# Performance work log

Measured on AMD Instinct MI355X. Metric: run time of the kernel, lower is better.

## Reference

```python
import jax, jax.numpy as jnp
import numpy as np

B, L = 16, 1024
D_MODEL, D_STATE, N_LAYERS = 256, 16, 2
FRAME_DIM, N_FRAMES, N_ACT = 115, 4, 19
GNN_H, GNN_K, ACT_EMB, GRID, N_PLAYERS = 32, 6, 16, 5, 22


def _ln(x, g, b, eps=1e-5):
    m = x.mean(-1, keepdims=True)
    v = ((x - m) ** 2).mean(-1, keepdims=True)
    return (x - m) / jnp.sqrt(v + eps) * g + b


def _kan(x, g, b, Wsp, Wbase, bias, beta):
    # x: [N, FRAME_DIM]
    grid = jnp.linspace(-1.0, 1.0, GRID)
    x = _ln(x, g, b)
    bta = jnp.clip(beta, 0.5, 6.0)
    basis = jnp.exp(-((x[..., None] - grid) ** 2) * bta)  # [N, I, G]
    # original: einsum('bdig,oid->bod').sum(-1) with basis dim d==1 broadcast
    # == sum over i, g (basis) and d (spline grid axis)
    spline = jnp.einsum('big,oid->bo', basis, Wsp)
    base = x @ Wbase.T
    return base + spline + bias


def _graph(fc, fp):
    # fc, fp: [N, 115] current / previous frame
    Bn = fc.shape[0]
    ball = fc[:, :2]
    lp = fc[:, 3:25].reshape(Bn, 11, 2)
    rp = fc[:, 25:47].reshape(Bn, 11, 2)
    lpp = fp[:, 3:25].reshape(Bn, 11, 2)
    rpp = fp[:, 25:47].reshape(Bn, 11, 2)
    pos = jnp.concatenate([lp, rp], 1)           # [N, 22, 2]
    posp = jnp.concatenate([lpp, rpp], 1)
    vel = pos - posp
    team = jnp.concatenate([jnp.zeros((Bn, 11, 1)), jnp.ones((Bn, 11, 1))], 1)
    bd = jnp.sqrt(((pos - ball[:, None, :]) ** 2).sum(-1, keepdims=True))
    prox = jnp.exp(-bd * 2)
    lc = lp.mean(1, keepdims=True)
    rc = rp.mean(1, keepdims=True)
    tc = jnp.concatenate([jnp.broadcast_to(lc, (Bn, 11, 2)),
                          jnp.broadcast_to(rc, (Bn, 11, 2))], 1)
    nodes = jnp.concatenate([pos, vel, team, prox, pos - tc], -1)  # [N, 22, 8]
    eye = jnp.eye(N_PLAYERS)
    d = jnp.sqrt(((pos[:, :, None, :] - pos[:, None, :, :]) ** 2).sum(-1)) + eye * 1e6
    _, idx = jax.lax.top_k(-d, GNN_K)
    adj = jax.nn.one_hot(idx, N_PLAYERS).sum(-2)
    adj = jnp.minimum(adj + eye, 1.0)
    adj = adj / jnp.clip(adj.sum(-1, keepdims=True), 1.0, None)
    # the torch model computes the graph under no_grad
    return jax.lax.stop_gradient(nodes), jax.lax.stop_gradient(adj)


def _s6(x, h0, lng, lnb, Win, Wdt, bdt, Alog, WB, WC, Dp, Wout):
    Bn, Ln, Dm = x.shape
    h0 = h0.reshape(Bn, Dm, D_STATE)
    xn = _ln(x, lng, lnb)
    xz = xn @ Win.T
    x_in, z = jnp.split(xz, 2, axis=-1)
    dt = jax.nn.softplus(x_in @ Wdt.T + bdt)     # [B, L, D]
    A = -jnp.exp(Alog)                            # [D, N]
    Bt = x_in @ WB.T                              # [B, L, N]
    Ct = x_in @ WC.T

    def step(h, inp):
        dt_t, x_t, B_t, C_t = inp                 # [B,D],[B,D],[B,N],[B,N]
        dA = jnp.exp(dt_t[:, :, None] * A)        # [B, D, N]
        h = dA * h + (dt_t * x_t)[:, :, None] * B_t[:, None, :]
        y = (h * C_t[:, None, :]).sum(-1)         # [B, D]
        return h, y

    hL, ys = jax.lax.scan(step, h0, (dt.swapaxes(0, 1), x_in.swapaxes(0, 1),
                                     Bt.swapaxes(0, 1), Ct.swapaxes(0, 1)))
    y = ys.swapaxes(0, 1)
    ssm = y * jax.nn.silu(z) + x_in * Dp
    return x + ssm @ Wout.T, hL.reshape(Bn, -1)


def setup_inputs() -> dict:
    key = jax.random.key(0)
    ks = iter(jax.random.split(key, 80))

    def nrm(shape, s=0.05):
        return jax.random.normal(next(ks), shape, dtype=jnp.float32) * s

    inp = {}
    inp['obs'] = jax.random.normal(next(ks), (B, L, N_FRAMES, FRAME_DIM), dtype=jnp.float32)
    inp['prev_actions'] = jax.random.randint(next(ks), (B, L), 0, N_ACT)
    inp['h0_0'] = jnp.zeros((B, D_MODEL * D_STATE), jnp.float32)
    inp['h0_1'] = jnp.zeros((B, D_MODEL * D_STATE), jnp.float32)
    inp['kan_ln_g'] = jnp.ones((FRAME_DIM,), jnp.float32)
    inp['kan_ln_b'] = jnp.zeros((FRAME_DIM,), jnp.float32)
    inp['kan_spline'] = nrm((D_MODEL, FRAME_DIM, GRID), 0.1)
    inp['kan_scale'] = jnp.ones((D_MODEL, FRAME_DIM), jnp.float32)
    inp['kan_bias'] = jnp.zeros((D_MODEL,), jnp.float32)
    inp['kan_beta'] = jnp.full((1,), 2.0, jnp.float32)
    inp['fn_g'] = jnp.ones((D_MODEL,), jnp.float32)
    inp['fn_b'] = jnp.zeros((D_MODEL,), jnp.float32)
    inp['gnn_W'] = nrm((GNN_H, 8))
    inp['edge_w'] = jnp.full((1,), 0.5, jnp.float32)
    inp['act_emb'] = nrm((N_ACT, ACT_EMB), 1.0)
    inp['W_ip'] = nrm((D_MODEL, D_MODEL + GNN_H + ACT_EMB))
    inp['b_ip'] = jnp.zeros((D_MODEL,), jnp.float32)
    for i in range(N_LAYERS):
        p = 'm%d_' % i
        inp[p + 'lng'] = jnp.ones((D_MODEL,), jnp.float32)
        inp[p + 'lnb'] = jnp.zeros((D_MODEL,), jnp.float32)
        inp[p + 'Win'] = nrm((2 * D_MODEL, D_MODEL))
        inp[p + 'Wdt'] = nrm((D_MODEL, D_MODEL))
        inp[p + 'bdt'] = jnp.zeros((D_MODEL,), jnp.float32)
        inp[p + 'Alog'] = jax.random.uniform(next(ks), (D_MODEL, D_STATE),
                                             minval=-3.0, maxval=-1.0, dtype=jnp.float32)
        inp[p + 'WB'] = nrm((D_STATE, D_MODEL))
        inp[p + 'WC'] = nrm((D_STATE, D_MODEL))
        inp[p + 'D'] = jnp.ones((D_MODEL,), jnp.float32)
        inp[p + 'Wout'] = nrm((D_MODEL, D_MODEL))
    inp['fl_g'] = jnp.ones((D_MODEL,), jnp.float32)
    inp['fl_b'] = jnp.zeros((D_MODEL,), jnp.float32)
    inp['pW1'] = nrm((128, D_MODEL)); inp['pb1'] = jnp.zeros((128,), jnp.float32)
    inp['pW2'] = nrm((N_ACT, 128)); inp['pb2'] = jnp.zeros((N_ACT,), jnp.float32)
    inp['vW1'] = nrm((64, D_MODEL)); inp['vb1'] = jnp.zeros((64,), jnp.float32)
    inp['vW2'] = nrm((1, 64)); inp['vb2'] = jnp.zeros((1,), jnp.float32)
    return inp


def reference(obs, prev_actions, h0_0, h0_1,
              kan_ln_g, kan_ln_b, kan_spline, kan_scale, kan_bias, kan_beta,
              fn_g, fn_b, gnn_W, edge_w, act_emb, W_ip, b_ip,
              m0_lng, m0_lnb, m0_Win, m0_Wdt, m0_bdt, m0_Alog, m0_WB, m0_WC, m0_D, m0_Wout,
              m1_lng, m1_lnb, m1_Win, m1_Wdt, m1_bdt, m1_Alog, m1_WB, m1_WC, m1_D, m1_Wout,
              fl_g, fl_b, pW1, pb1, pW2, pb2, vW1, vb1, vW2, vb2):
    BL = B * L
    # frame encoder (KAN) over all frames of all timesteps
    flat = obs.reshape(BL * N_FRAMES, FRAME_DIM)
    fe = _kan(flat, kan_ln_g, kan_ln_b, kan_spline, kan_scale, kan_bias, kan_beta)
    fe = jax.nn.relu(_ln(fe.reshape(BL, N_FRAMES, D_MODEL), fn_g, fn_b))
    feat = fe.mean(1)                                   # [BL, D]
    # GNN on last two frames
    fc = obs[:, :, -1, :].reshape(BL, FRAME_DIM)
    fp = obs[:, :, -2, :].reshape(BL, FRAME_DIM)
    nodes, adj = _graph(fc, fp)
    gx = nodes @ gnn_W.T                                # [BL, 22, H]
    agg = jnp.einsum('bij,bjd->bid', adj, gx)
    gx = gx * (1 - edge_w) + agg * edge_w
    gemb = gx.mean(1)                                   # [BL, H]
    aemb = act_emb[prev_actions].reshape(BL, ACT_EMB)
    x = jnp.concatenate([feat, gemb, aemb], -1) @ W_ip.T + b_ip
    x = x.reshape(B, L, D_MODEL)
    x, h1 = _s6(x, h0_0, m0_lng, m0_lnb, m0_Win, m0_Wdt, m0_bdt, m0_Alog, m0_WB, m0_WC, m0_D, m0_Wout)
    x, h2 = _s6(x, h0_1, m1_lng, m1_lnb, m1_Win, m1_Wdt, m1_bdt, m1_Alog, m1_WB, m1_WC, m1_D, m1_Wout)
    x = _ln(x, fl_g, fl_b)
    logits = jax.nn.relu(x @ pW1.T + pb1) @ pW2.T + pb2   # [B, L, N_ACT]
    value = (jax.nn.relu(x @ vW1.T + vb1) @ vW2.T + vb2)[..., 0]  # [B, L]
    return logits, value, h1, h2
```

## Files before the change

kernel.cpp:

```cpp
#include <hip/hip_runtime.h>
#include <math.h>

#define BB   16
#define LL   1024
#define BLR  (BB*LL)
#define DM   256
#define DS   16
#define FD   115
#define NF   4
#define NACTN 19
#define GH   32
#define GKN  6
#define AEM  16
#define NP   22
#define CATD 304
#define CATP 320
#define KKANP 256
#define KREALK 230
#define NC   16
#define CL   (LL/NC)
#define TT   16
#define LDK  40
#define XZW  800


typedef __attribute__((ext_vector_type(8))) short bf16x8;
typedef __attribute__((ext_vector_type(4))) float f32x4;

__device__ inline unsigned short f2bf(float f) {
    unsigned int u = __float_as_uint(f);
    u += 0x7fff + ((u >> 16) & 1);
    return (unsigned short)(u >> 16);
}
__device__ inline unsigned int f2bf2(float lo, float hi) {
    return (unsigned int)f2bf(lo) | ((unsigned int)f2bf(hi) << 16);
}
__device__ inline size_t swz(int row, int k) {
    return (size_t)(row >> 4)*4096 + (k >> 5)*512 + ((k >> 3) & 3)*128
         + (row & 15)*8 + (k & 7);
}

template<int NFRAG>
__global__ __launch_bounds__(256) void bgemm(
    const unsigned short* __restrict__ A, const unsigned short* __restrict__ W,
    const float* __restrict__ bias, float* __restrict__ C,
    int ldc, int act, int accum)
{
    const int tid = threadIdx.x;
    const int wid = tid >> 6, lane = tid & 63;
    const int wr = wid >> 1, wc = wid & 1;
    const int g = lane >> 4, r16 = lane & 15;
    const int bm = blockIdx.x * 64;
    const int bn = blockIdx.y * (NFRAG * 32);

    f32x4 acc[2][NFRAG] = {};
    const unsigned short* abase = A + ((size_t)(bm >> 4) + wr*2)*4096 + g*128 + r16*8;
    const unsigned short* wbase = W + ((size_t)(bn >> 4) + wc*NFRAG)*4096 + g*128 + r16*8;
    #pragma unroll
    for (int kk = 0; kk < 8; ++kk) {
        bf16x8 a0 = *(const bf16x8*)(abase + kk*512);
        bf16x8 a1 = *(const bf16x8*)(abase + 4096 + kk*512);
        bf16x8 bfr[NFRAG];
        #pragma unroll
        for (int ni = 0; ni < NFRAG; ++ni)
            bfr[ni] = *(const bf16x8*)(wbase + (size_t)ni*4096 + kk*512);
        #pragma unroll
        for (int ni = 0; ni < NFRAG; ++ni) {
            acc[0][ni] = __builtin_amdgcn_mfma_f32_16x16x32_bf16(a0, bfr[ni], acc[0][ni], 0,0,0);
            acc[1][ni] = __builtin_amdgcn_mfma_f32_16x16x32_bf16(a1, bfr[ni], acc[1][ni], 0,0,0);
        }
    }
    #pragma unroll
    for (int mi = 0; mi < 2; ++mi) {
        #pragma unroll
        for (int j = 0; j < 4; ++j) {
            int row = bm + wr*32 + mi*16 + g*4 + j;
            float* crow = C + (size_t)row * ldc;
            #pragma unroll
            for (int ni = 0; ni < NFRAG; ++ni) {
                int col = bn + wc*(NFRAG*16) + ni*16 + r16;
                float v = acc[mi][ni][j];
                if (act == 3) {
                    if (col >= 512 && col < 768) {
                        v += bias[col - 512];
                        v = fmaxf(v, 0.f) + __logf(1.f + __expf(-fabsf(v)));
                    }
                } else {
                    if (bias) v += bias[col];
                    if (act == 1) v = fmaxf(v, 0.f);
                }
                if (accum) v += crow[col];
                crow[col] = v;
            }
        }
    }
}

__global__ __launch_bounds__(256) void bgemm_ln(
    const unsigned short* __restrict__ A, const unsigned short* __restrict__ W,
    float* __restrict__ X, const float* __restrict__ g8p,
    const float* __restrict__ b8p, unsigned short* __restrict__ Y16)
{
    __shared__ float rsum[64][2];
    __shared__ float rsq[64][2];
    const int tid = threadIdx.x;
    const int bm = blockIdx.x * 64;
    const int wid = tid >> 6, lane = tid & 63;
    const int wr = wid >> 1, wc = wid & 1;
    const int g = lane >> 4, r16 = lane & 15;

    f32x4 acc[2][8] = {};
    const unsigned short* abase = A + ((size_t)(bm >> 4) + wr*2)*4096 + g*128 + r16*8;
    const unsigned short* wbase = W + (size_t)(wc*8)*4096 + g*128 + r16*8;
    #pragma unroll
    for (int kk = 0; kk < 8; ++kk) {
        bf16x8 a0 = *(const bf16x8*)(abase + kk*512);
        bf16x8 a1 = *(const bf16x8*)(abase + 4096 + kk*512);
        bf16x8 bfr[8];
        #pragma unroll
        for (int ni = 0; ni < 8; ++ni)
            bfr[ni] = *(const bf16x8*)(wbase + (size_t)ni*4096 + kk*512);
        #pragma unroll
        for (int ni = 0; ni < 8; ++ni) {
            acc[0][ni] = __builtin_amdgcn_mfma_f32_16x16x32_bf16(a0, bfr[ni], acc[0][ni], 0,0,0);
            acc[1][ni] = __builtin_amdgcn_mfma_f32_16x16x32_bf16(a1, bfr[ni], acc[1][ni], 0,0,0);
        }
    }
    #pragma unroll
    for (int mi = 0; mi < 2; ++mi) {
        #pragma unroll
        for (int j = 0; j < 4; ++j) {
            int row = bm + wr*32 + mi*16 + g*4 + j;
            float* xrow = X + (size_t)row * DM;
            float s = 0.f, q = 0.f;
            #pragma unroll
            for (int ni = 0; ni < 8; ++ni) {
                int col = wc*128 + ni*16 + r16;
                float v = acc[mi][ni][j] + xrow[col];
                acc[mi][ni][j] = v;
                xrow[col] = v;
                s += v; q += v*v;
            }
            #pragma unroll
            for (int off = 1; off < 16; off <<= 1) {
                s += __shfl_xor(s, off);
                q += __shfl_xor(q, off);
            }
            if (r16 == 0) {
                int lrow = wr*32 + mi*16 + g*4 + j;
                rsum[lrow][wc] = s; rsq[lrow][wc] = q;
            }
        }
    }
    __syncthreads();
    float g8[8], b8[8];
    #pragma unroll
    for (int ni = 0; ni < 8; ++ni) {
        int col = wc*128 + ni*16 + r16;
        g8[ni] = g8p[col]; b8[ni] = b8p[col];
    }
    #pragma unroll
    for (int mi = 0; mi < 2; ++mi) {
        #pragma unroll
        for (int j = 0; j < 4; ++j) {
            int lrow = wr*32 + mi*16 + g*4 + j;
            int row = bm + lrow;
            float sm = rsum[lrow][0] + rsum[lrow][1];
            float sq = rsq[lrow][0] + rsq[lrow][1];
            float mn = sm * (1.f/256.f);
            float var = fmaxf(sq * (1.f/256.f) - mn*mn, 0.f);
            float rstd = rsqrtf(var + 1e-5f);
            #pragma unroll
            for (int ni = 0; ni < 8; ++ni) {
                int col = wc*128 + ni*16 + r16;
                float v = (acc[mi][ni][j] - mn) * rstd * g8[ni] + b8[ni];
                Y16[swz(row, col)] = f2bf(v);
            }
        }
    }
}

__global__ __launch_bounds__(256) void mfma_gemm(
    const float* __restrict__ A, const unsigned short* __restrict__ W,
    const float* __restrict__ bias, float* __restrict__ C,
    int N, int Kp, int Kreal, int lda, int ldc, int act, int accum)
{
    __shared__ __align__(16) unsigned short As[128*LDK];
    __shared__ __align__(16) unsigned short Ws[128*LDK];
    const int tid = threadIdx.x;
    const int bm = blockIdx.x * 128;
    const int bn = blockIdx.y * 128;
    const int wid = tid >> 6, lane = tid & 63;
    const int wr = wid >> 1, wc = wid & 1;
    const int g = lane >> 4, r16 = lane & 15;
    const int srow = tid >> 1;
    const int shalf = (tid & 1) * 16;

    f32x4 acc[4][4] = {};
    for (int k0 = 0; k0 < Kp; k0 += 32) {
        uint4 alo = make_uint4(0u,0u,0u,0u), ahi = make_uint4(0u,0u,0u,0u);
        if (k0 + shalf < Kreal) {
            const float* ap = A + (size_t)(bm + srow) * lda + k0 + shalf;
            float4 a0 = *(const float4*)(ap);
            float4 a1 = *(const float4*)(ap + 4);
            float4 a2 = *(const float4*)(ap + 8);
            float4 a3 = *(const float4*)(ap + 12);
            alo = make_uint4(f2bf2(a0.x,a0.y), f2bf2(a0.z,a0.w),
                             f2bf2(a1.x,a1.y), f2bf2(a1.z,a1.w));
            ahi = make_uint4(f2bf2(a2.x,a2.y), f2bf2(a2.z,a2.w),
                             f2bf2(a3.x,a3.y), f2bf2(a3.z,a3.w));
        }
        unsigned short* ad = &As[srow*LDK + shalf];
        *(uint4*)(ad)     = alo;
        *(uint4*)(ad + 8) = ahi;
        int n = bn + srow;
        uint4 wv0 = make_uint4(0u,0u,0u,0u), wv1 = make_uint4(0u,0u,0u,0u);
        if (n < N) {
            const unsigned short* wp = W + (size_t)n * Kp + k0 + shalf;
            wv0 = ((const uint4*)wp)[0];
            wv1 = ((const uint4*)wp)[1];
        }
        unsigned short* wd = &Ws[srow*LDK + shalf];
        *(uint4*)(wd)     = wv0;
        *(uint4*)(wd + 8) = wv1;
        __syncthreads();

        bf16x8 af[4], bfr[4];
        #pragma unroll
        for (int mi = 0; mi < 4; ++mi)
            af[mi] = *reinterpret_cast<const bf16x8*>(&As[(wr*64 + mi*16 + r16)*LDK + g*8]);
        #pragma unroll
        for (int ni = 0; ni < 4; ++ni)
            bfr[ni] = *reinterpret_cast<const bf16x8*>(&Ws[(wc*64 + ni*16 + r16)*LDK + g*8]);
        #pragma unroll
        for (int mi = 0; mi < 4; ++mi)
            #pragma unroll
            for (int ni = 0; ni < 4; ++ni)
                acc[mi][ni] = __builtin_amdgcn_mfma_f32_16x16x32_bf16(
                    af[mi], bfr[ni], acc[mi][ni], 0, 0, 0);
        __syncthreads();
    }
    #pragma unroll
    for (int mi = 0; mi < 4; ++mi) {
        #pragma unroll
        for (int j = 0; j < 4; ++j) {
            int row = bm + wr*64 + mi*16 + g*4 + j;
            float* crow = C + (size_t)row * ldc;
            #pragma unroll
            for (int ni = 0; ni < 4; ++ni) {
                int col = bn + wc*64 + ni*16 + r16;
                if (col < N) {
                    float v = acc[mi][ni][j];
                    if (bias) v += bias[col];
                    if (accum) v += crow[col];
                    crow[col] = v;
                }
            }
        }
    }
}

__global__ __launch_bounds__(256) void kan_statgen(
    const float* __restrict__ obs, const float* __restrict__ lng,
    const float* __restrict__ lnb, const float* __restrict__ betap,
    unsigned short* __restrict__ AG)
{
    int row = blockIdx.x * 4 + (threadIdx.x >> 6);
    int l = threadIdx.x & 63;
    const float beta = fminf(fmaxf(betap[0], 0.5f), 6.0f);
    const float* o = obs + (size_t)row * FD;
    float v0 = o[l];
    float v1 = (l + 64 < FD) ? o[l + 64] : 0.f;
    float s = v0 + v1;
    for (int off = 32; off; off >>= 1) s += __shfl_xor(s, off);
    float m = s * (1.f / FD);
    float e0 = v0 - m;
    float e1 = (l + 64 < FD) ? (v1 - m) : 0.f;
    float ss = e0*e0 + e1*e1;
    for (int off = 32; off; off >>= 1) ss += __shfl_xor(ss, off);
    float rs = rsqrtf(ss * (1.f / FD) + 1e-5f);

    float x0 = e0 * rs * lng[l] + lnb[l];
    float sb0 = 0.f;
    #pragma unroll
    for (int g5 = 0; g5 < 5; ++g5) {
        float dx = x0 - (-1.f + 0.5f * (float)g5);
        sb0 += __expf(-dx*dx*beta);
    }
    unsigned int u0 = f2bf2(x0, sb0);
    unsigned int u1 = 0u;
    if (l + 64 < FD) {
        float x1 = e1 * rs * lng[l+64] + lnb[l+64];
        float sb1 = 0.f;
        #pragma unroll
        for (int g5 = 0; g5 < 5; ++g5) {
            float dx = x1 - (-1.f + 0.5f * (float)g5);
            sb1 += __expf(-dx*dx*beta);
        }
        u1 = f2bf2(x1, sb1);
    }
    size_t base = (size_t)(row >> 4) * 4096 + (row & 15) * 8
                + ((l >> 2) & 3) * 128 + ((2*l) & 7);
    *(unsigned int*)(AG + base + ((l >> 4)    ) * 512) = u0;
    *(unsigned int*)(AG + base + ((l >> 4) + 4) * 512) = u1;
}

__global__ void prep_wf16(const float* __restrict__ sp, const float* __restrict__ sc,
                          unsigned short* __restrict__ Wg)
{
    int idx = blockIdx.x * 256 + threadIdx.x;
    if (idx >= DM * KKANP) return;
    int o = idx >> 8, k = idx & 255;
    float v = 0.f;
    if (k < KREALK) {
        int i = k >> 1;
        if (k & 1) {
            const float* s5 = sp + ((size_t)o*FD + i)*5;
            v = s5[0] + s5[1] + s5[2] + s5[3] + s5[4];
        } else v = sc[o*FD + i];
    }
    Wg[swz(o, k)] = f2bf(v);
}

__global__ __launch_bounds__(256) void kan_gemm2(
    const unsigned short* __restrict__ AG, const unsigned short* __restrict__ WF,
    const float* __restrict__ kbias, const float* __restrict__ fng,
    const float* __restrict__ fnb, float* __restrict__ cat)
{
    __shared__ float rsum[64][2];
    __shared__ float rsq[64][2];
    const int tid = threadIdx.x;
    const int bm = blockIdx.x * 64;
    const int wid = tid >> 6, lane = tid & 63;
    const int wr = wid >> 1, wc = wid & 1;
    const int g = lane >> 4, r16 = lane & 15;

    f32x4 acc[2][8] = {};
    const unsigned short* abase = AG + ((size_t)(bm >> 4) + wr*2)*4096 + g*128 + r16*8;
    const unsigned short* wbase = WF + (size_t)(wc*8)*4096 + g*128 + r16*8;
    #pragma unroll
    for (int kk = 0; kk < 8; ++kk) {
        bf16x8 af0 = *(const bf16x8*)(abase + kk*512);
        bf16x8 af1 = *(const bf16x8*)(abase + 4096 + kk*512);
        bf16x8 bfr[8];
        #pragma unroll
        for (int ni = 0; ni < 8; ++ni)
            bfr[ni] = *(const bf16x8*)(wbase + (size_t)ni*4096 + kk*512);
        #pragma unroll
        for (int ni = 0; ni < 8; ++ni) {
            acc[0][ni] = __builtin_amdgcn_mfma_f32_16x16x32_bf16(af0, bfr[ni], acc[0][ni], 0,0,0);
            acc[1][ni] = __builtin_amdgcn_mfma_f32_16x16x32_bf16(af1, bfr[ni], acc[1][ni], 0,0,0);
        }
    }
    float bias8[8], g8[8], b8[8];
    #pragma unroll
    for (int ni = 0; ni < 8; ++ni) {
        int col = wc*128 + ni*16 + r16;
        bias8[ni] = kbias[col]; g8[ni] = fng[col]; b8[ni] = fnb[col];
    }
    #pragma unroll
    for (int mi = 0; mi < 2; ++mi) {
        #pragma unroll
        for (int j = 0; j < 4; ++j) {
            float s = 0.f, q = 0.f;
            #pragma unroll
            for (int ni = 0; ni < 8; ++ni) {
                float v = acc[mi][ni][j] + bias8[ni];
                s += v; q += v*v;
            }
            #pragma unroll
            for (int off = 1; off < 16; off <<= 1) {
                s += __shfl_xor(s, off);
                q += __shfl_xor(q, off);
            }
            if (r16 == 0) {
                int row = wr*32 + mi*16 + g*4 + j;
                rsum[row][wc] = s; rsq[row][wc] = q;
            }
        }
    }
    __syncthreads();
    #pragma unroll
    for (int mi = 0; mi < 2; ++mi) {
        int row0 = wr*32 + mi*16 + g*4;
        float o8[8] = {0.f,0.f,0.f,0.f,0.f,0.f,0.f,0.f};
        #pragma unroll
        for (int j = 0; j < 4; ++j) {
            int row = row0 + j;
            float sm = rsum[row][0] + rsum[row][1];
            float sq = rsq[row][0] + rsq[row][1];
            float mn = sm * (1.f/256.f);
            float var = fmaxf(sq * (1.f/256.f) - mn*mn, 0.f);
            float rstd = rsqrtf(var + 1e-5f);
            #pragma unroll
            for (int ni = 0; ni < 8; ++ni) {
                float v = acc[mi][ni][j] + bias8[ni];
                v = (v - mn) * rstd * g8[ni] + b8[ni];
                o8[ni] += fmaxf(v, 0.f);
            }
        }
        int rbl = (bm + row0) >> 2;
        float* crow = cat + (size_t)rbl * CATD;
        #pragma unroll
        for (int ni = 0; ni < 8; ++ni)
            crow[wc*128 + ni*16 + r16] = o8[ni] * 0.25f;
    }
}

__global__ __launch_bounds__(256) void gemm_f32(
    const float* __restrict__ A, const float* __restrict__ W,
    const float* __restrict__ bias, float* __restrict__ C,
    int N, int K, int lda, int ldc, int act, int accum)
{
    __shared__ float As[16][68];
    __shared__ float Ws[16][68];
    const int tid = threadIdx.x;
    const int bm = blockIdx.x * 64;
    const int bn = blockIdx.y * 64;
    const int ty = tid >> 4, tx = tid & 15;
    const int lr = tid >> 2;
    const int lk = (tid & 3) * 4;
    float acc[4][4] = {{0.f,0.f,0.f,0.f},{0.f,0.f,0.f,0.f},{0.f,0.f,0.f,0.f},{0.f,0.f,0.f,0.f}};

    for (int k0 = 0; k0 < K; k0 += 16) {
        float4 av = *reinterpret_cast<const float4*>(A + (size_t)(bm + lr) * lda + k0 + lk);
        As[lk+0][lr] = av.x; As[lk+1][lr] = av.y; As[lk+2][lr] = av.z; As[lk+3][lr] = av.w;
        float4 wv = make_float4(0.f, 0.f, 0.f, 0.f);
        if (bn + lr < N)
            wv = *reinterpret_cast<const float4*>(W + (size_t)(bn + lr) * K + k0 + lk);
        Ws[lk+0][lr] = wv.x; Ws[lk+1][lr] = wv.y; Ws[lk+2][lr] = wv.z; Ws[lk+3][lr] = wv.w;
        __syncthreads();
        #pragma unroll
        for (int kk = 0; kk < 16; ++kk) {
            float4 a4 = *reinterpret_cast<const float4*>(&As[kk][ty*4]);
            float4 b4 = *reinterpret_cast<const float4*>(&Ws[kk][tx*4]);
            float aa[4] = {a4.x, a4.y, a4.z, a4.w};
            float bb[4] = {b4.x, b4.y, b4.z, b4.w};
            #pragma unroll
            for (int i = 0; i < 4; ++i)
                #pragma unroll
                for (int j = 0; j < 4; ++j)
                    acc[i][j] = fmaf(aa[i], bb[j], acc[i][j]);
        }
        __syncthreads();
    }
    #pragma unroll
    for (int i = 0; i < 4; ++i) {
        int row = bm + ty*4 + i;
        #pragma unroll
        for (int j = 0; j < 4; ++j) {
            int col = bn + tx*4 + j;
            if (col < N) {
                float v = acc[i][j];
                if (bias) v += bias[col];
                if (act == 1) v = fmaxf(v, 0.f);
                size_t o = (size_t)row * ldc + col;
                if (accum) v += C[o];
                C[o] = v;
            }
        }
    }
}

__global__ void prep_bf16(const float* __restrict__ src, unsigned short* __restrict__ dst,
                          int N, int K, int Kp)
{
    int idx = blockIdx.x * 256 + threadIdx.x;
    if (idx >= N * Kp) return;
    int n = idx / Kp, k = idx - n * Kp;
    dst[idx] = (k < K) ? f2bf(src[(size_t)n * K + k]) : (unsigned short)0;
}

__global__ void prep_pv(const float* __restrict__ pW1, const float* __restrict__ vW1,
                        const float* __restrict__ pb1, const float* __restrict__ vb1,
                        unsigned short* __restrict__ PV16, float* __restrict__ PVB)
{
    int idx = blockIdx.x * 256 + threadIdx.x;
    if (idx < 192*256) {
        int n = idx >> 8, k = idx & 255;
        float v = (n < 128) ? pW1[(size_t)n*DM + k] : vW1[(size_t)(n-128)*DM + k];
        PV16[swz(n, k)] = f2bf(v);
    } else if (idx < 192*256 + 192) {
        int i = idx - 192*256;
        PVB[i] = (i < 128) ? pb1[i] : vb1[i-128];
    }
}

__global__ void prep_layerw(
    const float* __restrict__ Win, const float* __restrict__ WB,
    const float* __restrict__ WC, const float* __restrict__ Wdt,
    const float* __restrict__ Wout,
    unsigned short* __restrict__ WINX16, unsigned short* __restrict__ WOUT16)
{
    int idx = blockIdx.x * 256 + threadIdx.x;
    if (idx < 512*256) {
        int n = idx >> 8, k = idx & 255;
        WINX16[swz(n, k)] = f2bf(Win[idx]);
    } else if (idx < 768*256) {
        int j2 = idx - 512*256;
        int n = j2 >> 8, k = j2 & 255;
        const float* src = Wdt + (size_t)n*DM;
        float acc = 0.f;
        for (int j = 0; j < DM; ++j)
            acc = fmaf(src[j], Win[(size_t)j*DM + k], acc);
        WINX16[swz(512 + n, k)] = f2bf(acc);
    } else if (idx < 800*256) {
        int j2 = idx - 768*256;
        int n = j2 >> 8, k = j2 & 255;
        const float* src = (n < 16) ? (WB + n*DM) : (WC + (n-16)*DM);
        float acc = 0.f;
        for (int j = 0; j < DM; ++j)
            acc = fmaf(src[j], Win[(size_t)j*DM + k], acc);
        WINX16[swz(768 + n, k)] = f2bf(acc);
    } else if (idx < 800*256 + 256*256) {
        int j2 = idx - 800*256;
        int n = j2 >> 8, k = j2 & 255;
        WOUT16[swz(n, k)] = f2bf(Wout[j2]);
    }
}

__global__ __launch_bounds__(64) void graph_kernel(const float* __restrict__ obs,
    const float* __restrict__ gW, const float* __restrict__ ewp,
    float* __restrict__ out)
{
    __shared__ float px[NP], py[NP];
    __shared__ float nodes[NP][8];
    __shared__ float gxs[NP][GH];
    __shared__ unsigned int msk[NP];
    __shared__ float rden[NP];
    __shared__ float wgt[NP];
    const int row = blockIdx.x;
    const int lane = threadIdx.x;
    const float* fc = obs + ((size_t)row * NF + 3) * FD;
    const float* fp = obs + ((size_t)row * NF + 2) * FD;
    const float ew = ewp[0];

    if (lane < NP) {
        int i = lane;
        float p0, p1, q0, q1;
        if (i < 11) { p0 = fc[3+2*i];  p1 = fc[4+2*i];  q0 = fp[3+2*i];  q1 = fp[4+2*i]; }
        else { int ii = i-11; p0 = fc[25+2*ii]; p1 = fc[26+2*ii]; q0 = fp[25+2*ii]; q1 = fp[26+2*ii]; }
        px[i] = p0; py[i] = p1;
        float bx = fc[0], by = fc[1];
        float bd = sqrtf((p0-bx)*(p0-bx) + (p1-by)*(p1-by));
        nodes[i][0] = p0; nodes[i][1] = p1;
        nodes[i][2] = p0 - q0; nodes[i][3] = p1 - q1;
        nodes[i][4] = (i < 11) ? 0.f : 1.f;
        nodes[i][5] = __expf(-2.f * bd);
    }
    __syncthreads();
    if (lane < NP) {
        int base = (lane < 11) ? 0 : 11;
        float cx = 0.f, cy = 0.f;
        for (int j = 0; j < 11; ++j) { cx += px[base+j]; cy += py[base+j]; }
        cx *= (1.f/11.f); cy *= (1.f/11.f);
        nodes[lane][6] = px[lane] - cx;
        nodes[lane][7] = py[lane] - cy;
        unsigned sel = 0;
        for (int k = 0; k < GKN; ++k) {
            float best = 1e30f; int bj = 0;
            for (int j = 0; j < NP; ++j) {
                if (j == lane || ((sel >> j) & 1u)) continue;
                float dx = px[lane]-px[j], dy = py[lane]-py[j];
                float dd = sqrtf(dx*dx + dy*dy);
                if (dd < best) { best = dd; bj = j; }
            }
            sel |= (1u << bj);
        }
        unsigned full = sel | (1u << lane);
        msk[lane] = full;
        rden[lane] = 1.f / fmaxf((float)__popc(full), 1.f);
    }
    __syncthreads();
    for (int idx = lane; idx < NP*GH; idx += 64) {
        int i = idx >> 5, h = idx & 31;
        float s = 0.f;
        #pragma unroll
        for (int f = 0; f < 8; ++f) s += nodes[i][f] * gW[h*8 + f];
        gxs[i][h] = s;
    }
    __syncthreads();
    if (lane < NP) {
        float s = 0.f;
        for (int i = 0; i < NP; ++i) if ((msk[i] >> lane) & 1u) s += rden[i];
        wgt[lane] = (1.f - ew) + ew * s;
    }
    __syncthreads();
    if (lane < GH) {
        float s = 0.f;
        for (int j = 0; j < NP; ++j) s += wgt[j] * gxs[j][lane];
        out[(size_t)row * CATD + DM + lane] = s * (1.f/22.f);
    }
}

__global__ void gather_aemb(const int* __restrict__ pa, const float* __restrict__ emb,
                            float* __restrict__ out)
{
    int idx = blockIdx.x * 256 + threadIdx.x;
    int row = idx >> 4, e = idx & 15;
    out[(size_t)row * CATD + DM + GH + e] = emb[pa[row]*AEM + e];
}

__global__ __launch_bounds__(256) void ln256_swz(const float* __restrict__ X,
    const float* __restrict__ g, const float* __restrict__ b,
    unsigned short* __restrict__ Y16)
{
    int row = blockIdx.x * 4 + (threadIdx.x >> 6);
    int lane = threadIdx.x & 63;
    const float* x = X + (size_t)row * DM;
    float4 v = reinterpret_cast<const float4*>(x)[lane];
    float s = v.x + v.y + v.z + v.w;
    for (int off = 32; off; off >>= 1) s += __shfl_xor(s, off);
    float m = s * (1.f / DM);
    float d0 = v.x-m, d1 = v.y-m, d2 = v.z-m, d3 = v.w-m;
    float ss = d0*d0 + d1*d1 + d2*d2 + d3*d3;
    for (int off = 32; off; off >>= 1) ss += __shfl_xor(ss, off);
    float rstd = rsqrtf(ss * (1.f / DM) + 1e-5f);
    int c = lane * 4;
    float o0 = d0*rstd*g[c+0] + b[c+0];
    float o1 = d1*rstd*g[c+1] + b[c+1];
    float o2 = d2*rstd*g[c+2] + b[c+2];
    float o3 = d3*rstd*g[c+3] + b[c+3];
    size_t base = swz(row, c);
    *(uint2*)(Y16 + base) = make_uint2(f2bf2(o0, o1), f2bf2(o2, o3));
}

__global__ __launch_bounds__(256) void s6_chunkA(
    const float* __restrict__ xz, const float* __restrict__ Alog,
    float* __restrict__ P, float* __restrict__ S)
{
    __shared__ float sdt[TT][64], sx[TT][64];
    __shared__ __align__(16) float sB[TT][16];
    const int blk = blockIdx.x;
    const int dblk = blk & 3, c = (blk >> 2) & 15, b = blk >> 6;
    const int sg = threadIdx.x & 3, dl = threadIdx.x >> 2;
    const int d0 = dblk*64, d = d0 + dl;
    float A[4];
    #pragma unroll
    for (int k = 0; k < 4; ++k) A[k] = -__expf(Alog[d*DS + sg*4 + k]);
    const size_t r0 = (size_t)b*LL + c*CL;
    const int lt = threadIdx.x >> 4, lc = (threadIdx.x & 15) * 4;
    float Pv[4] = {1.f,1.f,1.f,1.f}, Sv[4] = {0.f,0.f,0.f,0.f};
    for (int t0 = 0; t0 < CL; t0 += TT) {
        size_t rb = r0 + t0 + lt;
        *(float4*)&sdt[lt][lc] = *(const float4*)(xz + rb*XZW + 512 + d0 + lc);
        *(float4*)&sx[lt][lc]  = *(const float4*)(xz + rb*XZW + d0 + lc);
        if (threadIdx.x < 64) {
            size_t rb2 = r0 + t0 + (threadIdx.x >> 2);
            *(float4*)&sB[threadIdx.x >> 2][(threadIdx.x & 3)*4] =
                *(const float4*)(xz + rb2*XZW + 768 + (threadIdx.x & 3)*4);
        }
        __syncthreads();
        #pragma unroll
        for (int tt = 0; tt < TT; ++tt) {
            float dtv = sdt[tt][dl];
            float u   = dtv * sx[tt][dl];
            float4 Bv = *(const float4*)&sB[tt][sg*4];
            float bb[4] = {Bv.x, Bv.y, Bv.z, Bv.w};
            #pragma unroll
            for (int k = 0; k < 4; ++k) {
                float dA = __expf(dtv * A[k]);
                Pv[k] *= dA;
                Sv[k] = fmaf(dA, Sv[k], u * bb[k]);
            }
        }
        __syncthreads();
    }
    size_t o = (((size_t)b*NC + c)*DM + d)*DS + sg*4;
    *(float4*)(P + o) = make_float4(Pv[0], Pv[1], Pv[2], Pv[3]);
    *(float4*)(S + o) = make_float4(Sv[0], Sv[1], Sv[2], Sv[3]);
}

__global__ __launch_bounds__(256) void s6_comb(
    const float* __restrict__ P, const float* __restrict__ S,
    const float* __restrict__ h0, float* __restrict__ hin, float* __restrict__ hout)
{
    int idx = blockIdx.x * 256 + threadIdx.x;
    int b = idx >> 12, ds = idx & 4095;
    float h = h0[idx];
    #pragma unroll
    for (int c = 0; c < NC; ++c) {
        size_t o = (((size_t)b*NC + c) << 12) + ds;
        hin[o] = h;
        h = fmaf(P[o], h, S[o]);
    }
    hout[idx] = h;
}

__global__ __launch_bounds__(256) void s6_chunkC(
    const float* __restrict__ xz, const float* __restrict__ Alog,
    const float* __restrict__ hin, const float* __restrict__ Dp,
    unsigned short* __restrict__ ssm16)
{
    __shared__ float sdt[TT][64], sx[TT][64], sz[TT][64];
    __shared__ __align__(16) float sB[TT][16], sC[TT][16];
    const int blk = blockIdx.x;
    const int dblk = blk & 3, c = (blk >> 2) & 15, b = blk >> 6;
    const int sg = threadIdx.x & 3, dl = threadIdx.x >> 2;
    const int d0 = dblk*64, d = d0 + dl;
    float A[4];
    #pragma unroll
    for (int k = 0; k < 4; ++k) A[k] = -__expf(Alog[d*DS + sg*4 + k]);
    const float Dv = Dp[d];
    const size_t r0 = (size_t)b*LL + c*CL;
    const int lt = threadIdx.x >> 4, lc = (threadIdx.x & 15) * 4;
    float4 h4 = *(const float4*)(hin + (((size_t)b*NC + c)*DM + d)*DS + sg*4);
    float h[4] = {h4.x, h4.y, h4.z, h4.w};
    for (int t0 = 0; t0 < CL; t0 += TT) {
        size_t rb = r0 + t0 + lt;
        *(float4*)&sdt[lt][lc] = *(const float4*)(xz + rb*XZW + 512 + d0 + lc);
        *(float4*)&sx[lt][lc]  = *(const float4*)(xz + rb*XZW + d0 + lc);
        *(float4*)&sz[lt][lc]  = *(const float4*)(xz + rb*XZW + 256 + d0 + lc);
        if (threadIdx.x < 128) {
            size_t rb2 = r0 + t0 + ((threadIdx.x & 63) >> 2);
            int col = (threadIdx.x & 3) * 4;
            if (threadIdx.x < 64)
                *(float4*)&sB[(threadIdx.x & 63) >> 2][col] =
                    *(const float4*)(xz + rb2*XZW + 768 + col);
            else
                *(float4*)&sC[(threadIdx.x & 63) >> 2][col] =
                    *(const float4*)(xz + rb2*XZW + 784 + col);
        }
        __syncthreads();
        #pragma unroll
        for (int tt = 0; tt < TT; ++tt) {
            float dtv = sdt[tt][dl];
            float xv  = sx[tt][dl];
            float u   = dtv * xv;
            float4 Bv = *(const float4*)&sB[tt][sg*4];
            float4 Cv = *(const float4*)&sC[tt][sg*4];
            float bb[4] = {Bv.x, Bv.y, Bv.z, Bv.w};
            float cc[4] = {Cv.x, Cv.y, Cv.z, Cv.w};
            float p = 0.f;
            #pragma unroll
            for (int k = 0; k < 4; ++k) {
                float dA = __expf(dtv * A[k]);
                h[k] = fmaf(dA, h[k], u * bb[k]);
                p = fmaf(h[k], cc[k], p);
            }
            p += __shfl_xor(p, 1);
            p += __shfl_xor(p, 2);
            if (sg == 0) {
                float zv = sz[tt][dl];
                float sil = zv / (1.f + __expf(-zv));
                int row = (int)(r0 + t0 + tt);
                ssm16[swz(row, d)] = f2bf(fmaf(p, sil, xv * Dv));
            }
        }
        __syncthreads();
    }
}

static inline void mgemm(hipStream_t st, const float* A, const unsigned short* W,
                         const float* bias, float* C, int M, int N, int Kp, int Kreal,
                         int lda, int ldc, int act, int accum) {
    dim3 g(M/128, (N+127)/128);
    mfma_gemm<<<g, 256, 0, st>>>(A, W, bias, C, N, Kp, Kreal, lda, ldc, act, accum);
}
static inline void gemm(hipStream_t st, const float* A, const float* W, const float* bias,
                        float* C, int M, int N, int K, int lda, int ldc, int act, int accum) {
    dim3 g(M/64, (N+63)/64);
    gemm_f32<<<g, 256, 0, st>>>(A, W, bias, C, N, K, lda, ldc, act, accum);
}

extern "C" void kernel_launch(void* const* d_in, const int* in_sizes, int n_in,
                              void* d_out, int out_size, void* d_ws, size_t ws_size,
                              hipStream_t stream) {
    (void)in_sizes; (void)n_in; (void)out_size; (void)ws_size;
    const float* obs      = (const float*)d_in[0];
    const int*   pa       = (const int*)d_in[1];
    const float* h0in[2]  = {(const float*)d_in[2], (const float*)d_in[3]};
    const float* kan_ln_g = (const float*)d_in[4];
    const float* kan_ln_b = (const float*)d_in[5];
    const float* kan_sp   = (const float*)d_in[6];
    const float* kan_sc   = (const float*)d_in[7];
    const float* kan_bias = (const float*)d_in[8];
    const float* kan_beta = (const float*)d_in[9];
    const float* fn_g     = (const float*)d_in[10];
    const float* fn_b     = (const float*)d_in[11];
    const float* gnn_W    = (const float*)d_in[12];
    const float* edge_w   = (const float*)d_in[13];
    const float* act_emb  = (const float*)d_in[14];
    const float* W_ip     = (const float*)d_in[15];
    const float* b_ip     = (const float*)d_in[16];
    const float* fl_g     = (const float*)d_in[37];
    const float* fl_b     = (const float*)d_in[38];
    const float* pW1      = (const float*)d_in[39];
    const float* pb1      = (const float*)d_in[40];
    const float* pW2      = (const float*)d_in[41];
    const float* pb2      = (const float*)d_in[42];
    const float* vW1      = (const float*)d_in[43];
    const float* vb1      = (const float*)d_in[44];
    const float* vW2      = (const float*)d_in[45];
    const float* vb2      = (const float*)d_in[46];

    const size_t SZ_BIG = (size_t)BLR * DM;
    float* ws = (float*)d_ws;
    float* X    = ws;
    float* R0   = X + SZ_BIG;
    unsigned short* XN16  = (unsigned short*)R0;
    unsigned short* SSM16 = XN16 + (size_t)BLR*DM;
    unsigned short* WIP16 = (unsigned short*)R0;
    unsigned short* WF16  = WIP16 + (size_t)DM*CATP;
    float* XZBC = R0 + SZ_BIG;
    unsigned short* AG16 = (unsigned short*)XZBC;
    float* R4   = XZBC + (size_t)BLR * XZW;
    const size_t CH = (size_t)BB * NC * DM * DS;
    float* Pbuf = R4;
    float* Sbuf = R4 + CH;
    float* HIN  = R4 + 2*CH;
    unsigned short* WINX16[2];
    WINX16[0] = (unsigned short*)(R4 + 3*CH);
    WINX16[1] = WINX16[0] + (size_t)XZW*DM;
    unsigned short* WOUT16[2];
    WOUT16[0] = WINX16[1] + (size_t)XZW*DM;
    WOUT16[1] = WOUT16[0] + DM*DM;
    unsigned short* PV16 = WOUT16[1] + DM*DM;
    float* PVB = (float*)(PV16 + 192*DM);

    float* out        = (float*)d_out;
    float* out_logits = out;
    float* out_value  = out + (size_t)BLR * NACTN;
    float* out_h[2]   = {out + (size_t)BLR*NACTN + BLR,
                         out + (size_t)BLR*NACTN + BLR + (size_t)BB*DM*DS};

    prep_wf16<<<(DM*KKANP+255)/256, 256, 0, stream>>>(kan_sp, kan_sc, WF16);
    prep_bf16<<<(DM*CATP+255)/256, 256, 0, stream>>>(W_ip, WIP16, DM, CATD, CATP);
    kan_statgen<<<BLR*NF/4, 256, 0, stream>>>(obs, kan_ln_g, kan_ln_b, kan_beta, AG16);
    kan_gemm2<<<BLR*NF/64, 256, 0, stream>>>(AG16, WF16, kan_bias, fn_g, fn_b, R4);
    graph_kernel<<<BLR, 64, 0, stream>>>(obs, gnn_W, edge_w, R4);
    gather_aemb<<<BLR*AEM/256, 256, 0, stream>>>(pa, act_emb, R4);

    mgemm(stream, R4, WIP16, b_ip, X, BLR, DM, CATP, CATD, CATD, DM, 0, 0);

    prep_pv<<<(192*256 + 192 + 255)/256, 256, 0, stream>>>(pW1, vW1, pb1, vb1, PV16, PVB);
    for (int l = 0; l < 2; ++l) {
        const float* Win  = (const float*)d_in[17 + 10*l + 2];
        const float* Wdt  = (const float*)d_in[17 + 10*l + 3];
        const float* WBp  = (const float*)d_in[17 + 10*l + 6];
        const float* WCp  = (const float*)d_in[17 + 10*l + 7];
        const float* Wout = (const float*)d_in[17 + 10*l + 9];
        prep_layerw<<<(800*256 + 256*256 + 255)/256, 256, 0, stream>>>(
            Win, WBp, WCp, Wdt, Wout, WINX16[l], WOUT16[l]);
    }

    ln256_swz<<<BLR/4, 256, 0, stream>>>(X, (const float*)d_in[17], (const float*)d_in[18], XN16);

    for (int l = 0; l < 2; ++l) {
        const float* bdt  = (const float*)d_in[17 + 10*l + 4];
        const float* Alog = (const float*)d_in[17 + 10*l + 5];
        const float* Dp   = (const float*)d_in[17 + 10*l + 8];
        const float* nlg  = (l == 0) ? (const float*)d_in[27] : fl_g;
        const float* nlb  = (l == 0) ? (const float*)d_in[28] : fl_b;

        bgemm<5><<<dim3(BLR/64, 5), 256, 0, stream>>>(
            XN16, WINX16[l], bdt, XZBC, XZW, 3, 0);
        s6_chunkA<<<BB*NC*4, 256, 0, stream>>>(XZBC, Alog, Pbuf, Sbuf);
        s6_comb<<<BB*DM*DS/256, 256, 0, stream>>>(Pbuf, Sbuf, h0in[l], HIN, out_h[l]);
        s6_chunkC<<<BB*NC*4, 256, 0, stream>>>(XZBC, Alog, HIN, Dp, SSM16);
        bgemm_ln<<<BLR/64, 256, 0, stream>>>(SSM16, WOUT16[l], X, nlg, nlb, XN16);
    }

    float* H = XZBC;
    bgemm<6><<<dim3(BLR/64, 1), 256, 0, stream>>>(XN16, PV16, PVB, H, 192, 1, 0);
    gemm(stream, H, pW2, pb2, out_logits, BLR, NACTN, 128, 192, NACTN, 0, 0);
    gemm(stream, H + 128, vW2, vb2, out_value, BLR, 1, 64, 192, 1, 0, 0);
}
```

Measured before the change: 368.9 us.

## Write concat features as swizzled bf16 and use bgemm for input projection

```diff
diff --git a/kernel.cpp b/kernel.cpp
--- a/kernel.cpp
+++ b/kernel.cpp
@@ -20,7 +20,6 @@
 #define NC   16
 #define CL   (LL/NC)
 #define TT   16
-#define LDK  40
 #define XZW  800
 
 
@@ -39,8 +38,12 @@
     return (size_t)(row >> 4)*4096 + (k >> 5)*512 + ((k >> 3) & 3)*128
          + (row & 15)*8 + (k & 7);
 }
-
-template<int NFRAG>
+__device__ inline size_t swz320(int row, int k) {
+    return (size_t)(row >> 4)*5120 + (k >> 5)*512 + ((k >> 3) & 3)*128
+         + (row & 15)*8 + (k & 7);
+}
+
+template<int NFRAG, int KFRAG>
 __global__ __launch_bounds__(256) void bgemm(
     const unsigned short* __restrict__ A, const unsigned short* __restrict__ W,
     const float* __restrict__ bias, float* __restrict__ C,
@@ -52,18 +55,19 @@
     const int g = lane >> 4, r16 = lane & 15;
     const int bm = blockIdx.x * 64;
     const int bn = blockIdx.y * (NFRAG * 32);
+    const int RB = KFRAG * 512;
 
     f32x4 acc[2][NFRAG] = {};
-    const unsigned short* abase = A + ((size_t)(bm >> 4) + wr*2)*4096 + g*128 + r16*8;
-    const unsigned short* wbase = W + ((size_t)(bn >> 4) + wc*NFRAG)*4096 + g*128 + r16*8;
-    #pragma unroll
-    for (int kk = 0; kk < 8; ++kk) {
+    const unsigned short* abase = A + ((size_t)(bm >> 4) + wr*2)*RB + g*128 + r16*8;
+    const unsigned short* wbase = W + ((size_t)(bn >> 4) + wc*NFRAG)*RB + g*128 + r16*8;
+    #pragma unroll
+    for (int kk = 0; kk < KFRAG; ++kk) {
         bf16x8 a0 = *(const bf16x8*)(abase + kk*512);
-        bf16x8 a1 = *(const bf16x8*)(abase + 4096 + kk*512);
+        bf16x8 a1 = *(const bf16x8*)(abase + RB + kk*512);
         bf16x8 bfr[NFRAG];
         #pragma unroll
         for (int ni = 0; ni < NFRAG; ++ni)
-            bfr[ni] = *(const bf16x8*)(wbase + (size_t)ni*4096 + kk*512);
+            bfr[ni] = *(const bf16x8*)(wbase + (size_t)ni*RB + kk*512);
         #pragma unroll
         for (int ni = 0; ni < NFRAG; ++ni) {
             acc[0][ni] = __builtin_amdgcn_mfma_f32_16x16x32_bf16(a0, bfr[ni], acc[0][ni], 0,0,0);
@@ -180,86 +184,6 @@
     }
 }
 
-__global__ __launch_bounds__(256) void mfma_gemm(
-    const float* __restrict__ A, const unsigned short* __restrict__ W,
-    const float* __restrict__ bias, float* __restrict__ C,
-    int N, int Kp, int Kreal, int lda, int ldc, int act, int accum)
-{
-    __shared__ __align__(16) unsigned short As[128*LDK];
-    __shared__ __align__(16) unsigned short Ws[128*LDK];
-    const int tid = threadIdx.x;
-    const int bm = blockIdx.x * 128;
-    const int bn = blockIdx.y * 128;
-    const int wid = tid >> 6, lane = tid & 63;
-    const int wr = wid >> 1, wc = wid & 1;
-    const int g = lane >> 4, r16 = lane & 15;
-    const int srow = tid >> 1;
-    const int shalf = (tid & 1) * 16;
-
-    f32x4 acc[4][4] = {};
-    for (int k0 = 0; k0 < Kp; k0 += 32) {
-        uint4 alo = make_uint4(0u,0u,0u,0u), ahi = make_uint4(0u,0u,0u,0u);
-        if (k0 + shalf < Kreal) {
-            const float* ap = A + (size_t)(bm + srow) * lda + k0 + shalf;
-            float4 a0 = *(const float4*)(ap);
-            float4 a1 = *(const float4*)(ap + 4);
-            float4 a2 = *(const float4*)(ap + 8);
-            float4 a3 = *(const float4*)(ap + 12);
-            alo = make_uint4(f2bf2(a0.x,a0.y), f2bf2(a0.z,a0.w),
-                             f2bf2(a1.x,a1.y), f2bf2(a1.z,a1.w));
-            ahi = make_uint4(f2bf2(a2.x,a2.y), f2bf2(a2.z,a2.w),
-                             f2bf2(a3.x,a3.y), f2bf2(a3.z,a3.w));
-        }
-        unsigned short* ad = &As[srow*LDK + shalf];
-        *(uint4*)(ad)     = alo;
-        *(uint4*)(ad + 8) = ahi;
-        int n = bn + srow;
-        uint4 wv0 = make_uint4(0u,0u,0u,0u), wv1 = make_uint4(0u,0u,0u,0u);
-        if (n < N) {
-            const unsigned short* wp = W + (size_t)n * Kp + k0 + shalf;
-            wv0 = ((const uint4*)wp)[0];
-            wv1 = ((const uint4*)wp)[1];
-        }
-        unsigned short* wd = &Ws[srow*LDK + shalf];
-        *(uint4*)(wd)     = wv0;
-        *(uint4*)(wd + 8) = wv1;
-        __syncthreads();
-
-        bf16x8 af[4], bfr[4];
-        #pragma unroll
-        for (int mi = 0; mi < 4; ++mi)
-            af[mi] = *reinterpret_cast<const bf16x8*>(&As[(wr*64 + mi*16 + r16)*LDK + g*8]);
-        #pragma unroll
-        for (int ni = 0; ni < 4; ++ni)
-            bfr[ni] = *reinterpret_cast<const bf16x8*>(&Ws[(wc*64 + ni*16 + r16)*LDK + g*8]);
-        #pragma unroll
-        for (int mi = 0; mi < 4; ++mi)
-            #pragma unroll
-            for (int ni = 0; ni < 4; ++ni)
-                acc[mi][ni] = __builtin_amdgcn_mfma_f32_16x16x32_bf16(
-                    af[mi], bfr[ni], acc[mi][ni], 0, 0, 0);
-        __syncthreads();
-    }
-    #pragma unroll
-    for (int mi = 0; mi < 4; ++mi) {
-        #pragma unroll
-        for (int j = 0; j < 4; ++j) {
-            int row = bm + wr*64 + mi*16 + g*4 + j;
-            float* crow = C + (size_t)row * ldc;
-            #pragma unroll
-            for (int ni = 0; ni < 4; ++ni) {
-                int col = bn + wc*64 + ni*16 + r16;
-                if (col < N) {
-                    float v = acc[mi][ni][j];
-                    if (bias) v += bias[col];
-                    if (accum) v += crow[col];
-                    crow[col] = v;
-                }
-            }
-        }
-    }
-}
-
 __global__ __launch_bounds__(256) void kan_statgen(
     const float* __restrict__ obs, const float* __restrict__ lng,
     const float* __restrict__ lnb, const float* __restrict__ betap,
@@ -305,27 +229,35 @@
     *(unsigned int*)(AG + base + ((l >> 4) + 4) * 512) = u1;
 }
 
-__global__ void prep_wf16(const float* __restrict__ sp, const float* __restrict__ sc,
-                          unsigned short* __restrict__ Wg)
+__global__ void prep_kanw(const float* __restrict__ sp, const float* __restrict__ sc,
+                          const float* __restrict__ W_ip,
+                          unsigned short* __restrict__ WF16,
+                          unsigned short* __restrict__ WIP320)
 {
     int idx = blockIdx.x * 256 + threadIdx.x;
-    if (idx >= DM * KKANP) return;
-    int o = idx >> 8, k = idx & 255;
-    float v = 0.f;
-    if (k < KREALK) {
-        int i = k >> 1;
-        if (k & 1) {
-            const float* s5 = sp + ((size_t)o*FD + i)*5;
-            v = s5[0] + s5[1] + s5[2] + s5[3] + s5[4];
-        } else v = sc[o*FD + i];
-    }
-    Wg[swz(o, k)] = f2bf(v);
+    if (idx < DM*KKANP) {
+        int o = idx >> 8, k = idx & 255;
+        float v = 0.f;
+        if (k < KREALK) {
+            int i = k >> 1;
+            if (k & 1) {
+                const float* s5 = sp + ((size_t)o*FD + i)*5;
+                v = s5[0] + s5[1] + s5[2] + s5[3] + s5[4];
+            } else v = sc[o*FD + i];
+        }
+        WF16[swz(o, k)] = f2bf(v);
+    } else if (idx < DM*KKANP + DM*CATP) {
+        int j = idx - DM*KKANP;
+        int o = j / CATP, k = j - o * CATP;
+        float v = (k < CATD) ? W_ip[(size_t)o*CATD + k] : 0.f;
+        WIP320[swz320(o, k)] = f2bf(v);
+    }
 }
 
 __global__ __launch_bounds__(256) void kan_gemm2(
     const unsigned short* __restrict__ AG, const unsigned short* __restrict__ WF,
     const float* __restrict__ kbias, const float* __restrict__ fng,
-    const float* __restrict__ fnb, float* __restrict__ cat)
+    const float* __restrict__ fnb, unsigned short* __restrict__ CAT16)
 {
     __shared__ float rsum[64][2];
     __shared__ float rsq[64][2];
@@ -400,10 +332,9 @@
             }
         }
         int rbl = (bm + row0) >> 2;
-        float* crow = cat + (size_t)rbl * CATD;
         #pragma unroll
         for (int ni = 0; ni < 8; ++ni)
-            crow[wc*128 + ni*16 + r16] = o8[ni] * 0.25f;
+            CAT16[swz320(rbl, wc*128 + ni*16 + r16)] = f2bf(o8[ni] * 0.25f);
     }
 }
 
@@ -462,37 +393,39 @@
     }
 }
 
-__global__ void prep_bf16(const float* __restrict__ src, unsigned short* __restrict__ dst,
-                          int N, int K, int Kp)
+__global__ void prep_layerw2(
+    const float* __restrict__ Win0, const float* __restrict__ WB0,
+    const float* __restrict__ WC0, const float* __restrict__ Wdt0,
+    const float* __restrict__ Wout0,
+    const float* __restrict__ Win1, const float* __restrict__ WB1,
+    const float* __restrict__ WC1, const float* __restrict__ Wdt1,
+    const float* __restrict__ Wout1,
+    const float* __restrict__ pW1, const float* __restrict__ vW1,
+    const float* __restrict__ pb1, const float* __restrict__ vb1,
+    unsigned short* __restrict__ WX0, unsigned short* __restrict__ WO0,
+    unsigned short* __restrict__ WX1, unsigned short* __restrict__ WO1,
+    unsigned short* __restrict__ PV16, float* __restrict__ PVB)
 {
     int idx = blockIdx.x * 256 + threadIdx.x;
-    if (idx >= N * Kp) return;
-    int n = idx / Kp, k = idx - n * Kp;
-    dst[idx] = (k < K) ? f2bf(src[(size_t)n * K + k]) : (unsigned short)0;
-}
-
-__global__ void prep_pv(const float* __restrict__ pW1, const float* __restrict__ vW1,
-                        const float* __restrict__ pb1, const float* __restrict__ vb1,
-                        unsigned short* __restrict__ PV16, float* __restrict__ PVB)
-{
-    int idx = blockIdx.x * 256 + threadIdx.x;
-    if (idx < 192*256) {
-        int n = idx >> 8, k = idx & 255;
-        float v = (n < 128) ? pW1[(size_t)n*DM + k] : vW1[(size_t)(n-128)*DM + k];
-        PV16[swz(n, k)] = f2bf(v);
-    } else if (idx < 192*256 + 192) {
-        int i = idx - 192*256;
-        PVB[i] = (i < 128) ? pb1[i] : vb1[i-128];
-    }
-}
-
-__global__ void prep_layerw(
-    const float* __restrict__ Win, const float* __restrict__ WB,
-    const float* __restrict__ WC, const float* __restrict__ Wdt,
-    const float* __restrict__ Wout,
-    unsigned short* __restrict__ WINX16, unsigned short* __restrict__ WOUT16)
-{
-    int idx = blockIdx.x * 256 + threadIdx.x;
+    int ly = blockIdx.y;
+    if (ly == 2) {
+        if (idx < 192*256) {
+            int n = idx >> 8, k = idx & 255;
+            float v = (n < 128) ? pW1[(size_t)n*DM + k] : vW1[(size_t)(n-128)*DM + k];
+            PV16[swz(n, k)] = f2bf(v);
+        } else if (idx < 192*256 + 192) {
+            int i = idx - 192*256;
+            PVB[i] = (i < 128) ? pb1[i] : vb1[i-128];
+        }
+        return;
+    }
+    const float* Win  = ly ? Win1 : Win0;
+    const float* WB   = ly ? WB1  : WB0;
+    const float* WC   = ly ? WC1  : WC0;
+    const float* Wdt  = ly ? Wdt1 : Wdt0;
+    const float* Wout = ly ? Wout1 : Wout0;
+    unsigned short* WINX16 = ly ? WX1 : WX0;
+    unsigned short* WOUT16 = ly ? WO1 : WO0;
     if (idx < 512*256) {
         int n = idx >> 8, k = idx & 255;
         WINX16[swz(n, k)] = f2bf(Win[idx]);
@@ -521,7 +454,7 @@
 
 __global__ __launch_bounds__(64) void graph_kernel(const float* __restrict__ obs,
     const float* __restrict__ gW, const float* __restrict__ ewp,
-    float* __restrict__ out)
+    unsigned short* __restrict__ CAT16)
 {
     __shared__ float px[NP], py[NP];
     __shared__ float nodes[NP][8];
@@ -589,16 +522,17 @@
     if (lane < GH) {
         float s = 0.f;
         for (int j = 0; j < NP; ++j) s += wgt[j] * gxs[j][lane];
-        out[(size_t)row * CATD + DM + lane] = s * (1.f/22.f);
-    }
-}
-
-__global__ void gather_aemb(const int* __restrict__ pa, const float* __restrict__ emb,
-                            float* __restrict__ out)
+        CAT16[swz320(row, DM + lane)] = f2bf(s * (1.f/22.f));
+    }
+}
+
+__global__ void gather_aemb32(const int* __restrict__ pa, const float* __restrict__ emb,
+                              unsigned short* __restrict__ CAT16)
 {
     int idx = blockIdx.x * 256 + threadIdx.x;
-    int row = idx >> 4, e = idx & 15;
-    out[(size_t)row * CATD + DM + GH + e] = emb[pa[row]*AEM + e];
+    int row = idx >> 5, e = idx & 31;
+    float v = (e < AEM) ? emb[pa[row]*AEM + e] : 0.f;
+    CAT16[swz320(row, DM + GH + e)] = f2bf(v);
 }
 
 __global__ __launch_bounds__(256) void ln256_swz(const float* __restrict__ X,
@@ -751,12 +685,6 @@
     }
 }
 
-static inline void mgemm(hipStream_t st, const float* A, const unsigned short* W,
-                         const float* bias, float* C, int M, int N, int Kp, int Kreal,
-                         int lda, int ldc, int act, int accum) {
-    dim3 g(M/128, (N+127)/128);
-    mfma_gemm<<<g, 256, 0, st>>>(A, W, bias, C, N, Kp, Kreal, lda, ldc, act, accum);
-}
 static inline void gemm(hipStream_t st, const float* A, const float* W, const float* bias,
                         float* C, int M, int N, int K, int lda, int ldc, int act, int accum) {
     dim3 g(M/64, (N+63)/64);
@@ -800,11 +728,12 @@
     float* R0   = X + SZ_BIG;
     unsigned short* XN16  = (unsigned short*)R0;
     unsigned short* SSM16 = XN16 + (size_t)BLR*DM;
-    unsigned short* WIP16 = (unsigned short*)R0;
-    unsigned short* WF16  = WIP16 + (size_t)DM*CATP;
+    unsigned short* WF16   = (unsigned short*)R0;
+    unsigned short* WIP320 = WF16 + (size_t)DM*KKANP;
     float* XZBC = R0 + SZ_BIG;
     unsigned short* AG16 = (unsigned short*)XZBC;
     float* R4   = XZBC + (size_t)BLR * XZW;
+    unsigned short* CAT16 = (unsigned short*)R4;
     const size_t CH = (size_t)BB * NC * DM * DS;
     float* Pbuf = R4;
     float* Sbuf = R4 + CH;
@@ -824,25 +753,22 @@
     float* out_h[2]   = {out + (size_t)BLR*NACTN + BLR,
                          out + (size_t)BLR*NACTN + BLR + (size_t)BB*DM*DS};
 
-    prep_wf16<<<(DM*KKANP+255)/256, 256, 0, stream>>>(kan_sp, kan_sc, WF16);
-    prep_bf16<<<(DM*CATP+255)/256, 256, 0, stream>>>(W_ip, WIP16, DM, CATD, CATP);
+    prep_kanw<<<(DM*KKANP + DM*CATP + 255)/256, 256, 0, stream>>>(
+        kan_sp, kan_sc, W_ip, WF16, WIP320);
     kan_statgen<<<BLR*NF/4, 256, 0, stream>>>(obs, kan_ln_g, kan_ln_b, kan_beta, AG16);
-    kan_gemm2<<<BLR*NF/64, 256, 0, stream>>>(AG16, WF16, kan_bias, fn_g, fn_b, R4);
-    graph_kernel<<<BLR, 64, 0, stream>>>(obs, gnn_W, edge_w, R4);
-    gather_aemb<<<BLR*AEM/256, 256, 0, stream>>>(pa, act_emb, R4);
-
-    mgemm(stream, R4, WIP16, b_ip, X, BLR, DM, CATP, CATD, CATD, DM, 0, 0);
-
-    prep_pv<<<(192*256 + 192 + 255)/256, 256, 0, stream>>>(pW1, vW1, pb1, vb1, PV16, PVB);
-    for (int l = 0; l < 2; ++l) {
-        const float* Win  = (const float*)d_in[17 + 10*l + 2];
-        const float* Wdt  = (const float*)d_in[17 + 10*l + 3];
-        const float* WBp  = (const float*)d_in[17 + 10*l + 6];
-        const float* WCp  = (const float*)d_in[17 + 10*l + 7];
-        const float* Wout = (const float*)d_in[17 + 10*l + 9];
-        prep_layerw<<<(800*256 + 256*256 + 255)/256, 256, 0, stream>>>(
-            Win, WBp, WCp, Wdt, Wout, WINX16[l], WOUT16[l]);
-    }
+    kan_gemm2<<<BLR*NF/64, 256, 0, stream>>>(AG16, WF16, kan_bias, fn_g, fn_b, CAT16);
+    graph_kernel<<<BLR, 64, 0, stream>>>(obs, gnn_W, edge_w, CAT16);
+    gather_aemb32<<<BLR*32/256, 256, 0, stream>>>(pa, act_emb, CAT16);
+
+    bgemm<8,10><<<dim3(BLR/64, 1), 256, 0, stream>>>(CAT16, WIP320, b_ip, X, DM, 0, 0);
+
+    prep_layerw2<<<dim3((800*256 + 256*256 + 255)/256, 3), 256, 0, stream>>>(
+        (const float*)d_in[19], (const float*)d_in[23], (const float*)d_in[24],
+        (const float*)d_in[20], (const float*)d_in[26],
+        (const float*)d_in[29], (const float*)d_in[33], (const float*)d_in[34],
+        (const float*)d_in[30], (const float*)d_in[36],
+        pW1, vW1, pb1, vb1,
+        WINX16[0], WOUT16[0], WINX16[1], WOUT16[1], PV16, PVB);
 
     ln256_swz<<<BLR/4, 256, 0, stream>>>(X, (const float*)d_in[17], (const float*)d_in[18], XN16);
 
@@ -853,7 +779,7 @@
         const float* nlg  = (l == 0) ? (const float*)d_in[27] : fl_g;
         const float* nlb  = (l == 0) ? (const float*)d_in[28] : fl_b;
 
-        bgemm<5><<<dim3(BLR/64, 5), 256, 0, stream>>>(
+        bgemm<5,8><<<dim3(BLR/64, 5), 256, 0, stream>>>(
             XN16, WINX16[l], bdt, XZBC, XZW, 3, 0);
         s6_chunkA<<<BB*NC*4, 256, 0, stream>>>(XZBC, Alog, Pbuf, Sbuf);
         s6_comb<<<BB*DM*DS/256, 256, 0, stream>>>(Pbuf, Sbuf, h0in[l], HIN, out_h[l]);
@@ -862,7 +788,7 @@
     }
 
     float* H = XZBC;
-    bgemm<6><<<dim3(BLR/64, 1), 256, 0, stream>>>(XN16, PV16, PVB, H, 192, 1, 0);
+    bgemm<6,8><<<dim3(BLR/64, 1), 256, 0, stream>>>(XN16, PV16, PVB, H, 192, 1, 0);
     gemm(stream, H, pW2, pb2, out_logits, BLR, NACTN, 128, 192, NACTN, 0, 0);
     gemm(stream, H + 128, vW2, vb2, out_value, BLR, 1, 64, 192, 1, 0, 0);
 }
```

Result: faster. 353.5 us, median of 2 (-4.2%).
